# Kernel optimization log

Hardware: AMD Instinct MI355X
Metric: run time of the kernel (lower is better)

## Reference

```python
import jax, jax.numpy as jnp
import numpy as np

V, MAXLEN, D, I, C, L, S = 32000, 4096, 1024, 4096, 1024, 4, 4096


def setup_inputs() -> dict:
    key = jax.random.key(0)
    ks = jax.random.split(key, 20)
    sd = 0.02
    inp = {
        "input_indices": jax.random.randint(ks[0], (S,), 0, V),
        "emb": jax.random.normal(ks[1], (V, D), jnp.float32) * sd,
        "pos": jax.random.normal(ks[2], (MAXLEN, D), jnp.float32) * sd,
        "Wq": jax.random.normal(ks[3], (L, D, I), jnp.float32) * sd,
        "bq": jnp.zeros((L, I), jnp.float32),
        "Wk": jax.random.normal(ks[4], (L, D, I), jnp.float32) * sd,
        "bk": jnp.zeros((L, I), jnp.float32),
        "Wv": jax.random.normal(ks[5], (L, D, I), jnp.float32) * sd,
        "bv": jnp.zeros((L, I), jnp.float32),
        "Wo": jax.random.normal(ks[6], (L, I, D), jnp.float32) * sd,
        "bo": jnp.zeros((L, D), jnp.float32),
        "W1": jax.random.normal(ks[7], (L, D, I), jnp.float32) * sd,
        "b1": jnp.zeros((L, I), jnp.float32),
        "W2": jax.random.normal(ks[8], (L, I, D), jnp.float32) * sd,
        "b2": jnp.zeros((L, D), jnp.float32),
        "Wout": jax.random.normal(ks[9], (D, C), jnp.float32) * sd,
        "bout": jnp.zeros((C,), jnp.float32),
    }
    return inp


def reference(input_indices, emb, pos, Wq, bq, Wk, bk, Wv, bv, Wo, bo, W1, b1, W2, b2, Wout, bout):
    s = input_indices.shape[0]
    x = emb[input_indices] + pos[:s]  # [S, D]
    causal_mask = jnp.triu(jnp.ones((s, s), bool), k=1)  # True above diagonal -> masked
    scale = 1.0 / np.sqrt(Wq.shape[-1]).astype(np.float32)

    def layer(x, p):
        wq, bq_, wk, bk_, wv, bv_, wo, bo_, w1, b1_, w2, b2_ = p
        q = x @ wq + bq_  # [S, I]
        k = x @ wk + bk_
        v = x @ wv + bv_
        scores = (q @ k.T) * scale  # [S, S]
        scores = jnp.where(causal_mask, -jnp.inf, scores)
        attn = jax.nn.softmax(scores, axis=-1)
        r = x + (attn @ v) @ wo + bo_  # residual + attention output projection
        f = jnp.maximum(r @ w1 + b1_, 0.0) @ w2 + b2_  # ReLU FFN
        return r + f, attn

    x, attention_maps = jax.lax.scan(
        layer, x, (Wq, bq, Wk, bk, Wv, bv, Wo, bo, W1, b1, W2, b2)
    )
    logits = x @ Wout + bout  # [S, C]
    log_probs = jax.nn.log_softmax(logits, axis=-1)
    return log_probs, attention_maps  # [S, C], [L, S, S]
```

## Files before the change

kernel.cpp:

```cpp
#include <hip/hip_runtime.h>
#include <stdint.h>
#include <math.h>

#define S_ 4096
#define D_ 1024
#define I_ 4096
#define C_ 1024
#define L_ 4

typedef unsigned short u16;
typedef short bf16x8 __attribute__((ext_vector_type(8)));
typedef float f32x4 __attribute__((ext_vector_type(4)));

__device__ __forceinline__ u16 f2bf(float f) {
  union { float f; uint32_t u; } c; c.f = f;
  return (u16)((c.u + 0x7FFFu + ((c.u >> 16) & 1u)) >> 16);
}

__device__ __forceinline__ void gll16(const void* g, void* l) {
  __builtin_amdgcn_global_load_lds(
      (__attribute__((address_space(1))) void*)(g),
      (__attribute__((address_space(3))) void*)(l), 16, 0, 0);
}

#define BAR() asm volatile("s_barrier" ::: "memory")
#define WAITV(n) asm volatile("s_waitcnt vmcnt(" #n ")" ::: "memory")

__device__ __forceinline__ int xcd_swz(int orig, int nwg) {
  int q8 = nwg >> 3, r8 = nwg & 7;
  int xcd = orig & 7, rem = orig >> 3;
  return (xcd < r8 ? xcd * (q8 + 1) : r8 * (q8 + 1) + (xcd - r8) * q8) + rem;
}

__device__ __forceinline__ void gemm256_body(
    u16* sA, u16* sB,
    const u16* __restrict__ A, const u16* __restrict__ Bt,
    const float* __restrict__ bias, const float* __restrict__ resid,
    float* __restrict__ outF, u16* __restrict__ outB,
    int N, int K, float scale, int relu,
    int row0, int col0, int t0, int t1)
{
  int tid = threadIdx.x, l = tid & 63;
  int w = tid >> 6;
  int wr = w >> 2, wc = w & 3;
  int lrow = l & 15, lq = l >> 4;
  int hb = wc >> 1;
  int rx = lrow & 7;

  const u16* ap[2]; const u16* bp[2]; int dst[2];
#pragma unroll
  for (int u = 0; u < 2; ++u) {
    int c = u * 512 + tid;
    int row = c >> 3;
    int oct = (c & 7) ^ (row & 7);
    ap[u] = A + (size_t)(row0 + row) * K + oct * 8;
    bp[u] = Bt + (size_t)(col0 + row) * K + oct * 8;
    dst[u] = c * 8;
  }

#define STAGE_A(par, hh, t)                                                     \
  { _Pragma("unroll") for (int u = 0; u < 2; ++u)                               \
      gll16(ap[u] + (size_t)(hh) * 128 * K + (t) * 64,                          \
            &sA[((par) * 2 + (hh)) * 8192 + dst[u]]); }
#define STAGE_B(par, hh, t)                                                     \
  { _Pragma("unroll") for (int u = 0; u < 2; ++u)                               \
      gll16(bp[u] + (size_t)(hh) * 128 * K + (t) * 64,                          \
            &sB[((par) * 2 + (hh)) * 8192 + dst[u]]); }
#define LD_A(DST, par, mh)                                                      \
  { _Pragma("unroll") for (int mi = 0; mi < 4; ++mi)                            \
    _Pragma("unroll") for (int kc = 0; kc < 2; ++kc)                            \
      DST[mi][kc] = *(const bf16x8*)&sA[((par) * 2 + wr) * 8192 +               \
          ((mh) * 64 + mi * 16 + lrow) * 64 + (((kc * 4 + lq) ^ rx) * 8)]; }
#define LD_B(DST, par, nh)                                                      \
  { _Pragma("unroll") for (int nj = 0; nj < 2; ++nj)                            \
    _Pragma("unroll") for (int kc = 0; kc < 2; ++kc)                            \
      DST[nj][kc] = *(const bf16x8*)&sB[((par) * 2 + hb) * 8192 +               \
          ((wc & 1) * 64 + (nh) * 32 + nj * 16 + lrow) * 64 +                   \
          (((kc * 4 + lq) ^ rx) * 8)]; }

  f32x4 acc[8][4];
#pragma unroll
  for (int i = 0; i < 8; ++i)
#pragma unroll
    for (int j = 0; j < 4; ++j) {
      acc[i][j][0] = 0.f; acc[i][j][1] = 0.f; acc[i][j][2] = 0.f; acc[i][j][3] = 0.f;
    }

#define MM(AF, MB, NB)                                                          \
  { __builtin_amdgcn_s_setprio(1);                                             \
    _Pragma("unroll") for (int kc = 0; kc < 2; ++kc)                            \
    _Pragma("unroll") for (int mi = 0; mi < 4; ++mi)                            \
    _Pragma("unroll") for (int nj = 0; nj < 2; ++nj)                            \
      acc[(MB) + mi][(NB) + nj] = __builtin_amdgcn_mfma_f32_16x16x32_bf16(      \
          AF[mi][kc], bfv[nj][kc], acc[(MB) + mi][(NB) + nj], 0, 0, 0);         \
    __builtin_amdgcn_s_setprio(0); }

  bf16x8 afA[4][2], afB[4][2], bfv[2][2];

  STAGE_A(0, 0, t0); STAGE_A(0, 1, t0); STAGE_B(0, 0, t0); STAGE_B(0, 1, t0);
  STAGE_A(1, 0, t0 + 1); STAGE_A(1, 1, t0 + 1); STAGE_B(1, 0, t0 + 1);
  WAITV(6);
  BAR();

  for (int t = t0; t < t1; ++t) {
    int p = (t - t0) & 1;
    LD_A(afA, p, 0);
    LD_B(bfv, p, 0);
    LD_A(afB, p, 1);
    if (t + 1 < t1) STAGE_B(p ^ 1, 1, t + 1);
    BAR();
    MM(afA, 0, 0);
    BAR();
    if (t + 2 < t1) STAGE_A(p, 0, t + 2);
    BAR();
    MM(afB, 4, 0);
    BAR();
    LD_B(bfv, p, 1);
    if (t + 2 < t1) STAGE_A(p, 1, t + 2);
    BAR();
    MM(afB, 4, 2);
    BAR();
    if (t + 2 < t1) STAGE_B(p, 0, t + 2);
    BAR();
    MM(afA, 0, 2);
    if (t + 2 < t1) { WAITV(6); } else { WAITV(0); }
    BAR();
  }
#undef STAGE_A
#undef STAGE_B
#undef LD_A
#undef LD_B
#undef MM

  float biasv[4] = {0.f, 0.f, 0.f, 0.f};
  if (bias) {
#pragma unroll
    for (int j = 0; j < 4; ++j) biasv[j] = bias[col0 + wc * 64 + j * 16 + lrow];
  }
#pragma unroll
  for (int i = 0; i < 8; ++i) {
#pragma unroll
    for (int r = 0; r < 4; ++r) {
      int row = row0 + wr * 128 + i * 16 + lq * 4 + r;
      size_t ro = (size_t)row * N;
#pragma unroll
      for (int j = 0; j < 4; ++j) {
        int col = col0 + wc * 64 + j * 16 + lrow;
        float v = acc[i][j][r] * scale + biasv[j];
        if (resid) v += resid[ro + col];
        if (relu) v = fmaxf(v, 0.f);
        if (outF) outF[ro + col] = v;
        if (outB) outB[ro + col] = f2bf(v);
      }
    }
  }
}

__global__ __launch_bounds__(512, 2) void gemm256k(
    const u16* __restrict__ A, const u16* __restrict__ Bt,
    const float* __restrict__ bias, const float* __restrict__ resid,
    float* __restrict__ outF, u16* __restrict__ outB,
    int M, int N, int K, float scale, int flags, int k0, int k1)
{
  extern __shared__ char smem[];
  int wg = xcd_swz(blockIdx.x, gridDim.x);
  int nbx = N / 256;
  int br = wg / nbx, bc = wg % nbx;
  gemm256_body((u16*)smem, (u16*)smem + 32768, A, Bt, bias, resid, outF, outB,
               N, K, scale, flags & 1, br * 256, bc * 256, k0 / 64, k1 / 64);
}

struct B3 { const float* b[3]; };
__global__ __launch_bounds__(512, 2) void gemm256_qkv(
    const u16* __restrict__ A, const u16* __restrict__ BtBase,
    B3 b3, u16* __restrict__ outBase, int K)
{
  extern __shared__ char smem[];
  int wg = xcd_swz(blockIdx.x, gridDim.x);
  int z = wg >> 8;
  int tile = wg & 255;
  int br = tile >> 4, bc = tile & 15;
  gemm256_body((u16*)smem, (u16*)smem + 32768, A,
               BtBase + (size_t)z * I_ * D_, b3.b[z], nullptr,
               nullptr, outBase + (size_t)z * S_ * I_,
               I_, K, 1.0f, 0, br * 256, bc * 256, 0, K / 64);
}

__global__ __launch_bounds__(512, 2) void gemm256_tri3(
    const u16* __restrict__ A, const u16* __restrict__ Bt,
    float* __restrict__ out0, float* __restrict__ out1, float* __restrict__ out2,
    int K, float scale)
{
  extern __shared__ char smem[];
  int wg = xcd_swz(blockIdx.x, gridDim.x);
  int ntri = gridDim.x / 3;
  int chunk = wg / ntri;
  int tile = wg - chunk * ntri;
  int br = (int)((sqrtf(8.0f * (float)tile + 1.0f) - 1.0f) * 0.5f);
  while ((br + 1) * (br + 2) / 2 <= tile) ++br;
  while (br * (br + 1) / 2 > tile) --br;
  int bc = tile - br * (br + 1) / 2;
  int t0 = (chunk == 0) ? 0 : (chunk == 1 ? 22 : 43);
  int t1 = (chunk == 0) ? 22 : (chunk == 1 ? 43 : 64);
  float* o = (chunk == 0) ? out0 : (chunk == 1 ? out1 : out2);
  gemm256_body((u16*)smem, (u16*)smem + 32768, A, Bt, nullptr, nullptr,
               o, nullptr, S_, K, scale, 0, br * 256, bc * 256, t0, t1);
}

__global__ __launch_bounds__(512, 2) void gemm256_pv(
    const u16* __restrict__ A, const u16* __restrict__ Bt,
    u16* __restrict__ outB, float* __restrict__ pv)
{
  extern __shared__ char smem[];
  int wg = xcd_swz(blockIdx.x, gridDim.x);
  if (wg < 128) {
    int br = wg >> 4, bc = wg & 15;
    gemm256_body((u16*)smem, (u16*)smem + 32768, A, Bt, nullptr, nullptr,
                 nullptr, outB, I_, S_, 1.0f, 0,
                 br * 256, bc * 256, 0, (br + 1) * 4);
  } else {
    int c = wg - 128;
    int br = 8 + (c >> 5);
    int bc = (c >> 1) & 15;
    int chunk = c & 1;
    int lim = (br + 1) * 4;
    int half = lim >> 1;
    float* o = pv + (size_t)chunk * (S_ / 2) * I_ - (size_t)2048 * I_;
    gemm256_body((u16*)smem, (u16*)smem + 32768, A, Bt, nullptr, nullptr,
                 o, nullptr, I_, S_, 1.0f, 0,
                 br * 256, bc * 256, chunk ? half : 0, chunk ? lim : half);
  }
}

__global__ __launch_bounds__(256) void combine2pv(
    const float* __restrict__ pv, u16* __restrict__ outB)
{
  const int MN = (S_ / 2) * I_;
  int i = (blockIdx.x * 256 + threadIdx.x) * 4;
  f32x4 v = *(const f32x4*)&pv[i];
  v += *(const f32x4*)&pv[MN + i];
  ushort4 b;
  b.x = f2bf(v[0]); b.y = f2bf(v[1]); b.z = f2bf(v[2]); b.w = f2bf(v[3]);
  *(ushort4*)&outB[(size_t)2048 * I_ + i] = b;
}

__global__ __launch_bounds__(512, 2) void gemm256_ks4(
    const u16* __restrict__ A, const u16* __restrict__ Bt,
    float* __restrict__ pOut, int M, int N, int K)
{
  extern __shared__ char smem[];
  int wg = xcd_swz(blockIdx.x, gridDim.x);
  int chunk = wg & 3;
  int tile = wg >> 2;
  int nbx = N / 256;
  int br = tile / nbx, bc = tile % nbx;
  float* o = pOut + (size_t)chunk * M * N;
  int kq = K / 4;
  gemm256_body((u16*)smem, (u16*)smem + 32768, A, Bt, nullptr, nullptr,
               o, nullptr, N, K, 1.0f, 0,
               br * 256, bc * 256, (chunk * kq) / 64, ((chunk + 1) * kq) / 64);
}

__global__ __launch_bounds__(256) void combine4(
    const float* __restrict__ p, const float* __restrict__ bias,
    const float* __restrict__ resid, float* __restrict__ outF,
    u16* __restrict__ outB, int MN, int N)
{
  int i = (blockIdx.x * 256 + threadIdx.x) * 4;
  f32x4 v = *(const f32x4*)&p[i];
  v += *(const f32x4*)&p[MN + i];
  v += *(const f32x4*)&p[2 * MN + i];
  v += *(const f32x4*)&p[3 * MN + i];
  int col = i & (N - 1);
  v += *(const f32x4*)&bias[col];
  v += *(const f32x4*)&resid[i];
  *(f32x4*)&outF[i] = v;
  ushort4 b;
  b.x = f2bf(v[0]); b.y = f2bf(v[1]); b.z = f2bf(v[2]); b.w = f2bf(v[3]);
  *(ushort4*)&outB[i] = b;
}

template <int BM_, int BN_>
__global__ __launch_bounds__(256) void gemm_bt(
    const u16* __restrict__ A, const u16* __restrict__ Bt,
    const float* __restrict__ bias, const float* __restrict__ resid,
    float* __restrict__ outF, u16* __restrict__ outB,
    int M, int N, int K, float scale, int flags)
{
  constexpr int FM = BM_ / 32;
  constexpr int FN = BN_ / 32;
  constexpr int ALOADS = BM_ * 8 / 256;
  constexpr int BLOADS = BN_ * 8 / 256;
  constexpr int WROWS = BM_ / 2;
  constexpr int WCOLS = BN_ / 2;

  int wg = xcd_swz(blockIdx.x, gridDim.x);
  int nbx = N / BN_;
  int br = wg / nbx, bc = wg % nbx;

  int tid = threadIdx.x;
  int l = tid & 63, w = tid >> 6;
  int wr = w >> 1, wc = w & 1;
  int lrow = l & 15, lq = l >> 4;
  int row0 = br * BM_, col0 = bc * BN_;

  __shared__ u16 lA[2][BM_ * 64];
  __shared__ u16 lB[2][BN_ * 64];

  const u16* aptr[ALOADS];
  const u16* bptr[BLOADS];
#pragma unroll
  for (int t = 0; t < ALOADS; ++t) {
    int c = t * 256 + tid;
    int row = c >> 3;
    int oct = (c & 7) ^ (row & 7);
    aptr[t] = A + (size_t)(row0 + row) * K + oct * 8;
  }
#pragma unroll
  for (int t = 0; t < BLOADS; ++t) {
    int c = t * 256 + tid;
    int row = c >> 3;
    int oct = (c & 7) ^ (row & 7);
    bptr[t] = Bt + (size_t)(col0 + row) * K + oct * 8;
  }

#define STAGE(b, koff)                                                          \
  {                                                                             \
    _Pragma("unroll") for (int t = 0; t < ALOADS; ++t)                          \
        gll16(aptr[t] + (koff), &lA[b][(t * 256 + tid) * 8]);                   \
    _Pragma("unroll") for (int t = 0; t < BLOADS; ++t)                          \
        gll16(bptr[t] + (koff), &lB[b][(t * 256 + tid) * 8]);                   \
  }

  f32x4 acc[FM][FN];
#pragma unroll
  for (int i = 0; i < FM; ++i)
#pragma unroll
    for (int j = 0; j < FN; ++j) {
      acc[i][j][0] = 0.f; acc[i][j][1] = 0.f; acc[i][j][2] = 0.f; acc[i][j][3] = 0.f;
    }

  int ktiles = K / 64;
  int rxA = lrow & 7;

  STAGE(0, 0);
  __syncthreads();
  int cur = 0;
  for (int kt = 0; kt < ktiles; ++kt) {
    if (kt + 1 < ktiles) STAGE(cur ^ 1, (kt + 1) * 64);
#pragma unroll
    for (int kc = 0; kc < 2; ++kc) {
      int kq = kc * 4 + lq;
      int octA = (kq ^ rxA) * 8;
      bf16x8 af[FM], bfv[FN];
#pragma unroll
      for (int i = 0; i < FM; ++i)
        af[i] = *(const bf16x8*)&lA[cur][(wr * WROWS + i * 16 + lrow) * 64 + octA];
#pragma unroll
      for (int j = 0; j < FN; ++j)
        bfv[j] = *(const bf16x8*)&lB[cur][(wc * WCOLS + j * 16 + lrow) * 64 + octA];
#pragma unroll
      for (int i = 0; i < FM; ++i)
#pragma unroll
        for (int j = 0; j < FN; ++j)
          acc[i][j] = __builtin_amdgcn_mfma_f32_16x16x32_bf16(af[i], bfv[j], acc[i][j], 0, 0, 0);
    }
    __syncthreads();
    cur ^= 1;
  }
#undef STAGE

  float biasv[FN];
#pragma unroll
  for (int j = 0; j < FN; ++j) biasv[j] = 0.f;
  if (bias) {
#pragma unroll
    for (int j = 0; j < FN; ++j) biasv[j] = bias[col0 + wc * WCOLS + j * 16 + lrow];
  }
  bool do_relu = (flags & 1) != 0;
#pragma unroll
  for (int i = 0; i < FM; ++i) {
#pragma unroll
    for (int r = 0; r < 4; ++r) {
      int row = row0 + wr * WROWS + i * 16 + lq * 4 + r;
      size_t ro = (size_t)row * N;
#pragma unroll
      for (int j = 0; j < FN; ++j) {
        int col = col0 + wc * WCOLS + j * 16 + lrow;
        float v = acc[i][j][r] * scale + biasv[j];
        if (resid) v += resid[ro + col];
        if (do_relu) v = fmaxf(v, 0.f);
        if (outF) outF[ro + col] = v;
        if (outB) outB[ro + col] = f2bf(v);
      }
    }
  }
}

struct T6 {
  const float* src[6];
  u16* dst[6];
};

__global__ __launch_bounds__(256) void trans6_f2b(T6 a) {
  __shared__ float tile[32][33];
  int z = blockIdx.z;
  bool big = (z == 3 || z == 5);
  int R = big ? I_ : D_;
  int C = big ? D_ : I_;
  int bid = blockIdx.y * gridDim.x + blockIdx.x;
  int nbx = C / 32;
  int bx = bid % nbx, by = bid / nbx;
  const float* src = a.src[z];
  u16* dst = a.dst[z];
  int c0 = bx * 32, r0 = by * 32;
  int tx = threadIdx.x & 31, ty = threadIdx.x >> 5;
#pragma unroll
  for (int i = 0; i < 32; i += 8)
    tile[ty + i][tx] = src[(size_t)(r0 + ty + i) * C + c0 + tx];
  __syncthreads();
#pragma unroll
  for (int i = 0; i < 32; i += 8)
    dst[(size_t)(c0 + ty + i) * R + r0 + tx] = f2bf(tile[tx][ty + i]);
}

__global__ __launch_bounds__(256) void trans_f2b(const float* __restrict__ src,
                                                 u16* __restrict__ dst, int R, int C)
{
  __shared__ float tile[32][33];
  int c0 = blockIdx.x * 32, r0 = blockIdx.y * 32;
  int tx = threadIdx.x & 31, ty = threadIdx.x >> 5;
#pragma unroll
  for (int i = 0; i < 32; i += 8)
    tile[ty + i][tx] = src[(size_t)(r0 + ty + i) * C + c0 + tx];
  __syncthreads();
#pragma unroll
  for (int i = 0; i < 32; i += 8)
    dst[(size_t)(c0 + ty + i) * R + r0 + tx] = f2bf(tile[tx][ty + i]);
}

__global__ __launch_bounds__(256) void trans_b2b(const u16* __restrict__ src,
                                                 u16* __restrict__ dst, int R, int C)
{
  __shared__ u16 tile[64][68];
  int c0 = blockIdx.x * 64, r0 = blockIdx.y * 64;
  int tx = threadIdx.x & 63, ty = threadIdx.x >> 6;
#pragma unroll
  for (int i = 0; i < 64; i += 4)
    tile[ty + i][tx] = src[(size_t)(r0 + ty + i) * C + c0 + tx];
  __syncthreads();
#pragma unroll
  for (int i = 0; i < 64; i += 4)
    dst[(size_t)(c0 + ty + i) * R + r0 + tx] = tile[tx][ty + i];
}

__global__ __launch_bounds__(256) void embed_k(const int* __restrict__ idx,
                                               const float* __restrict__ emb,
                                               const float* __restrict__ pos,
                                               float* __restrict__ xf, u16* __restrict__ xb)
{
  int s = blockIdx.y;
  int d = blockIdx.x * 256 + threadIdx.x;
  float v = emb[(size_t)idx[s] * D_ + d] + pos[(size_t)s * D_ + d];
  size_t o = (size_t)s * D_ + d;
  xf[o] = v;
  xb[o] = f2bf(v);
}

__global__ __launch_bounds__(256) void softmax_causal(float* __restrict__ att,
                                                      const float* __restrict__ attP1,
                                                      const float* __restrict__ attP2,
                                                      u16* __restrict__ attB)
{
  int s = blockIdx.x;
  __shared__ float row[S_];
  __shared__ float red[8];
  int tid = threadIdx.x, l = tid & 63, w = tid >> 6;
  int nv = s + 1;
  size_t base = (size_t)s * S_;
  float m = -3.0e38f;
  for (int c = tid; c < nv; c += 256) {
    float v = att[base + c] + attP1[base + c] + attP2[base + c];
    row[c] = v; m = fmaxf(m, v);
  }
#pragma unroll
  for (int off = 32; off; off >>= 1) m = fmaxf(m, __shfl_xor(m, off, 64));
  if (l == 0) red[w] = m;
  __syncthreads();
  m = fmaxf(fmaxf(red[0], red[1]), fmaxf(red[2], red[3]));
  float sum = 0.f;
  for (int c = tid; c < nv; c += 256) { float e = __expf(row[c] - m); row[c] = e; sum += e; }
#pragma unroll
  for (int off = 32; off; off >>= 1) sum += __shfl_xor(sum, off, 64);
  if (l == 0) red[4 + w] = sum;
  __syncthreads();
  sum = red[4] + red[5] + red[6] + red[7];
  float inv = 1.0f / sum;
  int nb = ((s >> 8) + 1) * 256;
  for (int c = tid; c < S_; c += 256) {
    float p = (c < nv) ? row[c] * inv : 0.0f;
    att[base + c] = p;
    if (c < nb) attB[base + c] = f2bf(p);
  }
}

__global__ __launch_bounds__(256) void logsoftmax_k(const float* __restrict__ logits,
                                                    float* __restrict__ out)
{
  int s = blockIdx.x;
  int tid = threadIdx.x, l = tid & 63, w = tid >> 6;
  __shared__ float red[8];
  size_t base = (size_t)s * C_;
  float v[4];
  float m = -3.0e38f;
#pragma unroll
  for (int k = 0; k < 4; ++k) { v[k] = logits[base + tid + k * 256]; m = fmaxf(m, v[k]); }
#pragma unroll
  for (int off = 32; off; off >>= 1) m = fmaxf(m, __shfl_xor(m, off, 64));
  if (l == 0) red[w] = m;
  __syncthreads();
  m = fmaxf(fmaxf(red[0], red[1]), fmaxf(red[2], red[3]));
  float sum = 0.f;
#pragma unroll
  for (int k = 0; k < 4; ++k) sum += __expf(v[k] - m);
#pragma unroll
  for (int off = 32; off; off >>= 1) sum += __shfl_xor(sum, off, 64);
  if (l == 0) red[4 + w] = sum;
  __syncthreads();
  sum = red[4] + red[5] + red[6] + red[7];
  float lz = logf(sum);
#pragma unroll
  for (int k = 0; k < 4; ++k) out[base + tid + k * 256] = v[k] - m - lz;
}

extern "C" void kernel_launch(void* const* d_in, const int* in_sizes, int n_in,
                              void* d_out, int out_size, void* d_ws, size_t ws_size,
                              hipStream_t stream) {
  (void)in_sizes; (void)n_in; (void)out_size; (void)ws_size;
  const int*   idx  = (const int*)d_in[0];
  const float* emb  = (const float*)d_in[1];
  const float* pos  = (const float*)d_in[2];
  const float* Wq   = (const float*)d_in[3];
  const float* bq   = (const float*)d_in[4];
  const float* Wk   = (const float*)d_in[5];
  const float* bk   = (const float*)d_in[6];
  const float* Wv   = (const float*)d_in[7];
  const float* bv   = (const float*)d_in[8];
  const float* Wo   = (const float*)d_in[9];
  const float* bo   = (const float*)d_in[10];
  const float* W1   = (const float*)d_in[11];
  const float* b1   = (const float*)d_in[12];
  const float* W2   = (const float*)d_in[13];
  const float* b2   = (const float*)d_in[14];
  const float* Wout = (const float*)d_in[15];
  const float* bout = (const float*)d_in[16];
  float* out = (float*)d_out;

  char* ws = (char*)d_ws;
  const size_t MB = 1024ull * 1024ull;
  float* xres  = (float*)(ws + 0);
  u16*  xbf    = (u16*)(ws + 16 * MB);
  u16*  bufQ   = (u16*)(ws + 24 * MB);
  u16*  bufK   = (u16*)(ws + 56 * MB);
  u16*  bufV   = (u16*)(ws + 88 * MB);
  u16*  bufVT  = (u16*)(ws + 120 * MB);
  u16*  attnB  = (u16*)(ws + 152 * MB);
  float* logit = (float*)(ws + 184 * MB);
  u16* WqT   = (u16*)(ws + 200 * MB);
  u16* WkT   = (u16*)(ws + 208 * MB);
  u16* WvT   = (u16*)(ws + 216 * MB);
  u16* WoT   = (u16*)(ws + 224 * MB);
  u16* W1T   = (u16*)(ws + 232 * MB);
  u16* W2T   = (u16*)(ws + 240 * MB);
  u16* WoutT = (u16*)(ws + 248 * MB);
  float* attP1 = (float*)(ws + 256 * MB);
  float* pK    = (float*)(ws + 320 * MB);

  const float iscale = 1.0f / 64.0f;
  const int LDSB = 131072;
  hipFuncSetAttribute((const void*)gemm256k,
                      hipFuncAttributeMaxDynamicSharedMemorySize, LDSB);
  hipFuncSetAttribute((const void*)gemm256_qkv,
                      hipFuncAttributeMaxDynamicSharedMemorySize, LDSB);
  hipFuncSetAttribute((const void*)gemm256_tri3,
                      hipFuncAttributeMaxDynamicSharedMemorySize, LDSB);
  hipFuncSetAttribute((const void*)gemm256_pv,
                      hipFuncAttributeMaxDynamicSharedMemorySize, LDSB);
  hipFuncSetAttribute((const void*)gemm256_ks4,
                      hipFuncAttributeMaxDynamicSharedMemorySize, LDSB);
  const int G_SQ = (S_ / 256) * (I_ / 256);

  embed_k<<<dim3(D_ / 256, S_), 256, 0, stream>>>(idx, emb, pos, xres, xbf);

  for (int layer = 0; layer < L_; ++layer) {
    T6 t6;
    t6.src[0] = Wq + (size_t)layer * D_ * I_; t6.dst[0] = WqT;
    t6.src[1] = Wk + (size_t)layer * D_ * I_; t6.dst[1] = WkT;
    t6.src[2] = Wv + (size_t)layer * D_ * I_; t6.dst[2] = WvT;
    t6.src[3] = Wo + (size_t)layer * I_ * D_; t6.dst[3] = WoT;
    t6.src[4] = W1 + (size_t)layer * D_ * I_; t6.dst[4] = W1T;
    t6.src[5] = W2 + (size_t)layer * I_ * D_; t6.dst[5] = W2T;
    trans6_f2b<<<dim3(128, 32, 6), 256, 0, stream>>>(t6);

    B3 b3;
    b3.b[0] = bq + (size_t)layer * I_;
    b3.b[1] = bk + (size_t)layer * I_;
    b3.b[2] = bv + (size_t)layer * I_;
    gemm256_qkv<<<3 * G_SQ, 512, LDSB, stream>>>(xbf, WqT, b3, bufQ, D_);

    trans_b2b<<<dim3(I_ / 64, S_ / 64), 256, 0, stream>>>(bufV, bufVT, S_, I_);

    float* attL = out + (size_t)S_ * C_ + (size_t)layer * S_ * S_;
    gemm256_tri3<<<3 * 136, 512, LDSB, stream>>>(bufQ, bufK, attL, attP1, pK,
                                                 I_, iscale);

    softmax_causal<<<S_, 256, 0, stream>>>(attL, attP1, pK, attnB);

    gemm256_pv<<<384, 512, LDSB, stream>>>(attnB, bufVT, bufQ, attP1);
    combine2pv<<<(S_ / 2) * (I_ / 1024), 256, 0, stream>>>(attP1, bufQ);

    gemm256_ks4<<<(S_ / 256) * (D_ / 256) * 4, 512, LDSB, stream>>>(
        bufQ, WoT, pK, S_, D_, I_);
    combine4<<<(S_ * D_) / 1024, 256, 0, stream>>>(
        pK, bo + (size_t)layer * D_, xres, xres, xbf, S_ * D_, D_);

    gemm256k<<<G_SQ, 512, LDSB, stream>>>(
        xbf, W1T, b1 + (size_t)layer * I_, nullptr, nullptr, bufK,
        S_, I_, D_, 1.0f, 1, 0, D_);

    gemm256_ks4<<<(S_ / 256) * (D_ / 256) * 4, 512, LDSB, stream>>>(
        bufK, W2T, pK, S_, D_, I_);
    combine4<<<(S_ * D_) / 1024, 256, 0, stream>>>(
        pK, b2 + (size_t)layer * D_, xres, xres, xbf, S_ * D_, D_);
  }

  trans_f2b<<<dim3(C_ / 32, D_ / 32), 256, 0, stream>>>(Wout, WoutT, D_, C_);
  gemm_bt<64, 128><<<(S_ / 64) * (C_ / 128), 256, 0, stream>>>(
      xbf, WoutT, bout, nullptr, logit, nullptr, S_, C_, D_, 1.0f, 0);
  logsoftmax_k<<<S_, 256, 0, stream>>>(logit, out);
}
```

Before: 2.283 ms.

## Store split-K partial sums in fp16 instead of fp32

Partial results of the split-K GEMMs (QK^T chunks, PV halves, Wo/W2 k-split partials) are now written as fp16 instead of fp32, and the combine and softmax kernels read and convert them. This halves the memory traffic of the intermediate partial buffers and adds a separate buffer for the first QK chunk rather than writing it into the output. The cost is lost precision in the partial sums and fp16 range limits on intermediates.

```diff
diff --git a/kernel.cpp b/kernel.cpp
--- a/kernel.cpp
+++ b/kernel.cpp
@@ -17,6 +17,15 @@
   return (u16)((c.u + 0x7FFFu + ((c.u >> 16) & 1u)) >> 16);
 }
 
+__device__ __forceinline__ u16 f2h(float f) {
+  _Float16 h = (_Float16)f;
+  return *(u16*)&h;
+}
+__device__ __forceinline__ float h2f(u16 b) {
+  _Float16 h = *(_Float16*)&b;
+  return (float)h;
+}
+
 __device__ __forceinline__ void gll16(const void* g, void* l) {
   __builtin_amdgcn_global_load_lds(
       (__attribute__((address_space(1))) void*)(g),
@@ -36,7 +45,7 @@
     u16* sA, u16* sB,
     const u16* __restrict__ A, const u16* __restrict__ Bt,
     const float* __restrict__ bias, const float* __restrict__ resid,
-    float* __restrict__ outF, u16* __restrict__ outB,
+    float* __restrict__ outF, u16* __restrict__ outB, u16* __restrict__ outH,
     int N, int K, float scale, int relu,
     int row0, int col0, int t0, int t1)
 {
@@ -151,6 +160,7 @@
         if (relu) v = fmaxf(v, 0.f);
         if (outF) outF[ro + col] = v;
         if (outB) outB[ro + col] = f2bf(v);
+        if (outH) outH[ro + col] = f2h(v);
       }
     }
   }
@@ -167,7 +177,8 @@
   int nbx = N / 256;
   int br = wg / nbx, bc = wg % nbx;
   gemm256_body((u16*)smem, (u16*)smem + 32768, A, Bt, bias, resid, outF, outB,
-               N, K, scale, flags & 1, br * 256, bc * 256, k0 / 64, k1 / 64);
+               nullptr, N, K, scale, flags & 1, br * 256, bc * 256,
+               k0 / 64, k1 / 64);
 }
 
 struct B3 { const float* b[3]; };
@@ -182,13 +193,13 @@
   int br = tile >> 4, bc = tile & 15;
   gemm256_body((u16*)smem, (u16*)smem + 32768, A,
                BtBase + (size_t)z * I_ * D_, b3.b[z], nullptr,
-               nullptr, outBase + (size_t)z * S_ * I_,
+               nullptr, outBase + (size_t)z * S_ * I_, nullptr,
                I_, K, 1.0f, 0, br * 256, bc * 256, 0, K / 64);
 }
 
 __global__ __launch_bounds__(512, 2) void gemm256_tri3(
     const u16* __restrict__ A, const u16* __restrict__ Bt,
-    float* __restrict__ out0, float* __restrict__ out1, float* __restrict__ out2,
+    u16* __restrict__ out0, u16* __restrict__ out1, u16* __restrict__ out2,
     int K, float scale)
 {
   extern __shared__ char smem[];
@@ -202,21 +213,21 @@
   int bc = tile - br * (br + 1) / 2;
   int t0 = (chunk == 0) ? 0 : (chunk == 1 ? 22 : 43);
   int t1 = (chunk == 0) ? 22 : (chunk == 1 ? 43 : 64);
-  float* o = (chunk == 0) ? out0 : (chunk == 1 ? out1 : out2);
+  u16* o = (chunk == 0) ? out0 : (chunk == 1 ? out1 : out2);
   gemm256_body((u16*)smem, (u16*)smem + 32768, A, Bt, nullptr, nullptr,
-               o, nullptr, S_, K, scale, 0, br * 256, bc * 256, t0, t1);
+               nullptr, nullptr, o, S_, K, scale, 0, br * 256, bc * 256, t0, t1);
 }
 
 __global__ __launch_bounds__(512, 2) void gemm256_pv(
     const u16* __restrict__ A, const u16* __restrict__ Bt,
-    u16* __restrict__ outB, float* __restrict__ pv)
+    u16* __restrict__ outB, u16* __restrict__ pvH)
 {
   extern __shared__ char smem[];
   int wg = xcd_swz(blockIdx.x, gridDim.x);
   if (wg < 128) {
     int br = wg >> 4, bc = wg & 15;
     gemm256_body((u16*)smem, (u16*)smem + 32768, A, Bt, nullptr, nullptr,
-                 nullptr, outB, I_, S_, 1.0f, 0,
+                 nullptr, outB, nullptr, I_, S_, 1.0f, 0,
                  br * 256, bc * 256, 0, (br + 1) * 4);
   } else {
     int c = wg - 128;
@@ -225,28 +236,31 @@
     int chunk = c & 1;
     int lim = (br + 1) * 4;
     int half = lim >> 1;
-    float* o = pv + (size_t)chunk * (S_ / 2) * I_ - (size_t)2048 * I_;
+    u16* o = pvH + (size_t)chunk * (S_ / 2) * I_ - (size_t)2048 * I_;
     gemm256_body((u16*)smem, (u16*)smem + 32768, A, Bt, nullptr, nullptr,
-                 o, nullptr, I_, S_, 1.0f, 0,
+                 nullptr, nullptr, o, I_, S_, 1.0f, 0,
                  br * 256, bc * 256, chunk ? half : 0, chunk ? lim : half);
   }
 }
 
 __global__ __launch_bounds__(256) void combine2pv(
-    const float* __restrict__ pv, u16* __restrict__ outB)
+    const u16* __restrict__ pvH, u16* __restrict__ outB)
 {
   const int MN = (S_ / 2) * I_;
   int i = (blockIdx.x * 256 + threadIdx.x) * 4;
-  f32x4 v = *(const f32x4*)&pv[i];
-  v += *(const f32x4*)&pv[MN + i];
-  ushort4 b;
-  b.x = f2bf(v[0]); b.y = f2bf(v[1]); b.z = f2bf(v[2]); b.w = f2bf(v[3]);
-  *(ushort4*)&outB[(size_t)2048 * I_ + i] = b;
+  ushort4 a = *(const ushort4*)&pvH[i];
+  ushort4 b = *(const ushort4*)&pvH[MN + i];
+  ushort4 o;
+  o.x = f2bf(h2f(a.x) + h2f(b.x));
+  o.y = f2bf(h2f(a.y) + h2f(b.y));
+  o.z = f2bf(h2f(a.z) + h2f(b.z));
+  o.w = f2bf(h2f(a.w) + h2f(b.w));
+  *(ushort4*)&outB[(size_t)2048 * I_ + i] = o;
 }
 
 __global__ __launch_bounds__(512, 2) void gemm256_ks4(
     const u16* __restrict__ A, const u16* __restrict__ Bt,
-    float* __restrict__ pOut, int M, int N, int K)
+    u16* __restrict__ pOut, int M, int N, int K)
 {
   extern __shared__ char smem[];
   int wg = xcd_swz(blockIdx.x, gridDim.x);
@@ -254,30 +268,35 @@
   int tile = wg >> 2;
   int nbx = N / 256;
   int br = tile / nbx, bc = tile % nbx;
-  float* o = pOut + (size_t)chunk * M * N;
+  u16* o = pOut + (size_t)chunk * M * N;
   int kq = K / 4;
   gemm256_body((u16*)smem, (u16*)smem + 32768, A, Bt, nullptr, nullptr,
-               o, nullptr, N, K, 1.0f, 0,
+               nullptr, nullptr, o, N, K, 1.0f, 0,
                br * 256, bc * 256, (chunk * kq) / 64, ((chunk + 1) * kq) / 64);
 }
 
 __global__ __launch_bounds__(256) void combine4(
-    const float* __restrict__ p, const float* __restrict__ bias,
+    const u16* __restrict__ p, const float* __restrict__ bias,
     const float* __restrict__ resid, float* __restrict__ outF,
     u16* __restrict__ outB, int MN, int N)
 {
   int i = (blockIdx.x * 256 + threadIdx.x) * 4;
-  f32x4 v = *(const f32x4*)&p[i];
-  v += *(const f32x4*)&p[MN + i];
-  v += *(const f32x4*)&p[2 * MN + i];
-  v += *(const f32x4*)&p[3 * MN + i];
+  ushort4 a = *(const ushort4*)&p[i];
+  ushort4 b = *(const ushort4*)&p[MN + i];
+  ushort4 c = *(const ushort4*)&p[2 * MN + i];
+  ushort4 d = *(const ushort4*)&p[3 * MN + i];
+  f32x4 v;
+  v[0] = h2f(a.x) + h2f(b.x) + h2f(c.x) + h2f(d.x);
+  v[1] = h2f(a.y) + h2f(b.y) + h2f(c.y) + h2f(d.y);
+  v[2] = h2f(a.z) + h2f(b.z) + h2f(c.z) + h2f(d.z);
+  v[3] = h2f(a.w) + h2f(b.w) + h2f(c.w) + h2f(d.w);
   int col = i & (N - 1);
   v += *(const f32x4*)&bias[col];
   v += *(const f32x4*)&resid[i];
   *(f32x4*)&outF[i] = v;
-  ushort4 b;
-  b.x = f2bf(v[0]); b.y = f2bf(v[1]); b.z = f2bf(v[2]); b.w = f2bf(v[3]);
-  *(ushort4*)&outB[i] = b;
+  ushort4 o;
+  o.x = f2bf(v[0]); o.y = f2bf(v[1]); o.z = f2bf(v[2]); o.w = f2bf(v[3]);
+  *(ushort4*)&outB[i] = o;
 }
 
 template <int BM_, int BN_>
@@ -468,8 +487,9 @@
 }
 
 __global__ __launch_bounds__(256) void softmax_causal(float* __restrict__ att,
-                                                      const float* __restrict__ attP1,
-                                                      const float* __restrict__ attP2,
+                                                      const u16* __restrict__ p0,
+                                                      const u16* __restrict__ p1,
+                                                      const u16* __restrict__ p2,
                                                       u16* __restrict__ attB)
 {
   int s = blockIdx.x;
@@ -480,7 +500,7 @@
   size_t base = (size_t)s * S_;
   float m = -3.0e38f;
   for (int c = tid; c < nv; c += 256) {
-    float v = att[base + c] + attP1[base + c] + attP2[base + c];
+    float v = h2f(p0[base + c]) + h2f(p1[base + c]) + h2f(p2[base + c]);
     row[c] = v; m = fmaxf(m, v);
   }
 #pragma unroll
@@ -573,8 +593,10 @@
   u16* W1T   = (u16*)(ws + 232 * MB);
   u16* W2T   = (u16*)(ws + 240 * MB);
   u16* WoutT = (u16*)(ws + 248 * MB);
-  float* attP1 = (float*)(ws + 256 * MB);
-  float* pK    = (float*)(ws + 320 * MB);
+  u16* attP0 = (u16*)(ws + 256 * MB);
+  u16* attP1 = (u16*)(ws + 288 * MB);
+  u16* attP2 = (u16*)(ws + 320 * MB);
+  u16* shP   = (u16*)(ws + 352 * MB);
 
   const float iscale = 1.0f / 64.0f;
   const int LDSB = 131072;
@@ -611,27 +633,27 @@
     trans_b2b<<<dim3(I_ / 64, S_ / 64), 256, 0, stream>>>(bufV, bufVT, S_, I_);
 
     float* attL = out + (size_t)S_ * C_ + (size_t)layer * S_ * S_;
-    gemm256_tri3<<<3 * 136, 512, LDSB, stream>>>(bufQ, bufK, attL, attP1, pK,
+    gemm256_tri3<<<3 * 136, 512, LDSB, stream>>>(bufQ, bufK, attP0, attP1, attP2,
                                                  I_, iscale);
 
-    softmax_causal<<<S_, 256, 0, stream>>>(attL, attP1, pK, attnB);
-
-    gemm256_pv<<<384, 512, LDSB, stream>>>(attnB, bufVT, bufQ, attP1);
-    combine2pv<<<(S_ / 2) * (I_ / 1024), 256, 0, stream>>>(attP1, bufQ);
+    softmax_causal<<<S_, 256, 0, stream>>>(attL, attP0, attP1, attP2, attnB);
+
+    gemm256_pv<<<384, 512, LDSB, stream>>>(attnB, bufVT, bufQ, shP);
+    combine2pv<<<(S_ / 2) * (I_ / 1024), 256, 0, stream>>>(shP, bufQ);
 
     gemm256_ks4<<<(S_ / 256) * (D_ / 256) * 4, 512, LDSB, stream>>>(
-        bufQ, WoT, pK, S_, D_, I_);
+        bufQ, WoT, shP, S_, D_, I_);
     combine4<<<(S_ * D_) / 1024, 256, 0, stream>>>(
-        pK, bo + (size_t)layer * D_, xres, xres, xbf, S_ * D_, D_);
+        shP, bo + (size_t)layer * D_, xres, xres, xbf, S_ * D_, D_);
 
     gemm256k<<<G_SQ, 512, LDSB, stream>>>(
         xbf, W1T, b1 + (size_t)layer * I_, nullptr, nullptr, bufK,
         S_, I_, D_, 1.0f, 1, 0, D_);
 
     gemm256_ks4<<<(S_ / 256) * (D_ / 256) * 4, 512, LDSB, stream>>>(
-        bufK, W2T, pK, S_, D_, I_);
+        bufK, W2T, shP, S_, D_, I_);
     combine4<<<(S_ * D_) / 1024, 256, 0, stream>>>(
-        pK, b2 + (size_t)layer * D_, xres, xres, xbf, S_ * D_, D_);
+        shP, b2 + (size_t)layer * D_, xres, xres, xbf, S_ * D_, D_);
   }
 
   trans_f2b<<<dim3(C_ / 32, D_ / 32), 256, 0, stream>>>(Wout, WoutT, D_, C_);
```

After: 2.181 ms. -4.5%, faster.
